# Optimization experiments

Measured on AMD Instinct MI355X. Metric: run time of the kernel, lower is better.

The kernel has to match this reference:

```python
import jax, jax.numpy as jnp
import numpy as np


def _adaptive_pool_mat(n_in, n_out):
    # torch AdaptiveAvgPool2d bin edges: start=floor(i*n_in/n_out), end=ceil((i+1)*n_in/n_out)
    M = np.zeros((n_out, n_in), np.float32)
    for i in range(n_out):
        s = (i * n_in) // n_out
        e = -(-((i + 1) * n_in) // n_out)
        M[i, s:e] = 1.0 / (e - s)
    return jnp.asarray(M)


def _bilinear_mat(n_out, n_in):
    # torch F.interpolate bilinear, align_corners=False, as a (n_out, n_in) matrix
    M = np.zeros((n_out, n_in), np.float32)
    scale = n_in / n_out
    for i in range(n_out):
        src = max((i + 0.5) * scale - 0.5, 0.0)
        i0 = min(int(np.floor(src)), n_in - 1)
        w = src - i0
        i1 = min(i0 + 1, n_in - 1)
        M[i, i0] += 1.0 - w
        M[i, i1] += w
    return jnp.asarray(M)


def _bn(x, g, b, m, v):
    # inference-mode BatchNorm2d over channel axis 1 of (B,C,H,W)
    inv = g / jnp.sqrt(v + 1e-5)
    return x * inv[None, :, None, None] + (b - m * inv)[None, :, None, None]


def _selective_scan(u, delta, A, Bs, Cs, D):
    # u, delta: (B,K,Di,L); A: (K,Di,N); Bs, Cs: (B,K,N,L); D: (K,Di)
    def step(h, inp):
        u_l, d_l, B_l, C_l = inp  # (B,K,Di), (B,K,Di), (B,K,N), (B,K,N)
        h = h * jnp.exp(d_l[..., None] * A) + (d_l * u_l)[..., None] * B_l[:, :, None, :]
        return h, jnp.einsum('bkdn,bkn->bkd', h, C_l)

    h0 = jnp.zeros(u.shape[:3] + (A.shape[-1],), u.dtype)
    xs = (u.transpose(3, 0, 1, 2), delta.transpose(3, 0, 1, 2),
          Bs.transpose(3, 0, 1, 2), Cs.transpose(3, 0, 1, 2))
    _, ys = jax.lax.scan(step, h0, xs)  # ys: (L,B,K,Di)
    return ys.transpose(1, 2, 3, 0) + D[None, :, :, None] * u


def _ss2d(x, in_proj_w, conv_w, conv_b, x_proj_w, dt_w, dt_b, A_logs, Ds, ln_g, ln_b, out_proj_w):
    # x: (B,H,W,d_model); VMamba SS2D with K=4 scan directions
    B, H, W, _ = x.shape
    K, N = 4, 16
    R = dt_w.shape[-1]
    Di = in_proj_w.shape[0] // 2
    xz = jnp.einsum('bhwc,ec->bhwe', x, in_proj_w)
    xi, z = jnp.split(xz, 2, axis=-1)
    xc = xi.transpose(0, 3, 1, 2)  # (B,Di,H,W)
    xc = jax.lax.conv_general_dilated(xc, conv_w, (1, 1), [(1, 1), (1, 1)],
                                      dimension_numbers=('NCHW', 'OIHW', 'NCHW'),
                                      feature_group_count=Di)
    xc = jax.nn.silu(xc + conv_b[None, :, None, None])
    L = H * W
    x_hw = xc.reshape(B, Di, L)
    x_wh = xc.transpose(0, 1, 3, 2).reshape(B, Di, L)
    xs2 = jnp.stack([x_hw, x_wh], axis=1)
    xs4 = jnp.concatenate([xs2, jnp.flip(xs2, axis=-1)], axis=1)  # (B,4,Di,L)
    x_dbl = jnp.einsum('bkdl,kcd->bkcl', xs4, x_proj_w)
    dts, Bm, Cm = jnp.split(x_dbl, [R, R + N], axis=2)
    delta = jax.nn.softplus(jnp.einsum('bkrl,kdr->bkdl', dts, dt_w) + dt_b[None, :, :, None])
    A = -jnp.exp(A_logs).reshape(K, Di, N)
    out_y = _selective_scan(xs4, delta, A, Bm, Cm, Ds.reshape(K, Di))  # (B,4,Di,L)
    inv_y = jnp.flip(out_y[:, 2:4], axis=-1)
    wh_y = out_y[:, 1].reshape(B, Di, W, H).transpose(0, 1, 3, 2).reshape(B, Di, L)
    invwh_y = inv_y[:, 1].reshape(B, Di, W, H).transpose(0, 1, 3, 2).reshape(B, Di, L)
    y = out_y[:, 0] + inv_y[:, 0] + wh_y + invwh_y  # (B,Di,L)
    y = y.transpose(0, 2, 1).reshape(B, H, W, Di)
    mu = jnp.mean(y, -1, keepdims=True)
    var = jnp.var(y, -1, keepdims=True)
    y = (y - mu) / jnp.sqrt(var + 1e-5) * ln_g + ln_b  # out_norm (LayerNorm)
    y = y * jax.nn.silu(z)
    return jnp.einsum('bhwd,cd->bhwc', y, out_proj_w)


def _forward(x, pool_w, pool_b, bn_g, bn_b, bn_m, bn_v, in_proj_w, conv_w, conv_b,
             x_proj_w, dt_w, dt_b, A_logs, Ds, ln_g, ln_b, out_proj_w,
             cbr_w, cbr_b, cbr_g, cbr_beta, cbr_m, cbr_v):
    B, C, H, W = x.shape
    pool_scales = [1, 5, 9, 13]  # generate_arithmetic_sequence(1, 16, 4)
    outs = [x]
    # pool layer 0: conv1x1 -> BN -> ReLU -> global avg pool -> upsample (constant)
    y0 = jnp.einsum('bchw,dc->bdhw', x, pool_w[0]) + pool_b[0][None, :, None, None]
    y0 = jax.nn.relu(_bn(y0, bn_g[0], bn_b[0], bn_m[0], bn_v[0]))
    y0 = jnp.mean(y0, axis=(2, 3), keepdims=True)
    outs.append(jnp.broadcast_to(y0, (B, y0.shape[1], H, W)))
    # pool layers 1..3: adaptive avg pool -> conv1x1 -> BN -> ReLU -> bilinear upsample
    for i, s in enumerate(pool_scales[1:], start=1):
        Mh, Mw = _adaptive_pool_mat(H, s), _adaptive_pool_mat(W, s)
        p = jnp.einsum('bchw,ph,qw->bcpq', x, Mh, Mw)
        p = jnp.einsum('bcpq,dc->bdpq', p, pool_w[i]) + pool_b[i][None, :, None, None]
        p = jax.nn.relu(_bn(p, bn_g[i], bn_b[i], bn_m[i], bn_v[i]))
        Uh, Uw = _bilinear_mat(H, s), _bilinear_mat(W, s)
        outs.append(jnp.einsum('bcpq,hp,wq->bchw', p, Uh, Uw))
    feat = jnp.concatenate(outs, axis=1)  # (B, dim*4 + in_chs = 1024, H, W)
    y = _ss2d(feat.transpose(0, 2, 3, 1), in_proj_w, conv_w, conv_b, x_proj_w,
              dt_w, dt_b, A_logs, Ds, ln_g, ln_b, out_proj_w)
    y = y.transpose(0, 3, 1, 2)
    # cbr: conv1x1 -> BN -> GELU
    y = jnp.einsum('bchw,dc->bdhw', y, cbr_w) + cbr_b[None, :, None, None]
    y = _bn(y, cbr_g, cbr_beta, cbr_m, cbr_v)
    return jax.nn.gelu(y, approximate=False)


def setup_inputs():
    key = jax.random.key(0)
    ks = jax.random.split(key, 20)
    B, C, H, W = 4, 512, 16, 16
    dim, P = 128, 4
    dm = dim * P + C            # 1024
    Di, K, N, R = 2 * dm, 4, 16, dm // 16  # 2048, 4, 16, 64
    f = jax.random.normal
    return {
        'x': f(ks[0], (B, C, H, W), jnp.float32),
        'pool_w': f(ks[1], (P, dim, C), jnp.float32) * 0.05,
        'pool_b': f(ks[2], (P, dim), jnp.float32) * 0.05,
        'bn_g': jnp.ones((P, dim), jnp.float32),
        'bn_b': jnp.zeros((P, dim), jnp.float32),
        'bn_m': f(ks[3], (P, dim), jnp.float32) * 0.1,
        'bn_v': jax.random.uniform(ks[4], (P, dim), jnp.float32, 0.5, 1.5),
        'in_proj_w': f(ks[5], (2 * Di, dm), jnp.float32) * 0.02,
        'conv_w': f(ks[6], (Di, 1, 3, 3), jnp.float32) * 0.1,
        'conv_b': f(ks[7], (Di,), jnp.float32) * 0.05,
        'x_proj_w': f(ks[8], (K, R + 2 * N, Di), jnp.float32) * 0.02,
        'dt_w': f(ks[9], (K, Di, R), jnp.float32) * 0.05,
        'dt_b': f(ks[10], (K, Di), jnp.float32) * 0.1,
        'A_logs': jax.random.uniform(ks[11], (K * Di, N), jnp.float32),
        'Ds': f(ks[12], (K * Di,), jnp.float32) * 0.1,
        'ln_g': jnp.ones((Di,), jnp.float32),
        'ln_b': jnp.zeros((Di,), jnp.float32),
        'out_proj_w': f(ks[13], (dm, Di), jnp.float32) * 0.02,
        'cbr_w': f(ks[14], (dim, dm), jnp.float32) * 0.05,
        'cbr_b': f(ks[15], (dim,), jnp.float32) * 0.05,
        'cbr_g': jnp.ones((dim,), jnp.float32),
        'cbr_beta': jnp.zeros((dim,), jnp.float32),
        'cbr_m': f(ks[16], (dim,), jnp.float32) * 0.1,
        'cbr_v': jax.random.uniform(ks[17], (dim,), jnp.float32, 0.5, 1.5),
    }


def reference(x, pool_w, pool_b, bn_g, bn_b, bn_m, bn_v, in_proj_w, conv_w, conv_b,
              x_proj_w, dt_w, dt_b, A_logs, Ds, ln_g, ln_b, out_proj_w,
              cbr_w, cbr_b, cbr_g, cbr_beta, cbr_m, cbr_v):
    return _forward(x, pool_w, pool_b, bn_g, bn_b, bn_m, bn_v, in_proj_w, conv_w, conv_b,
                    x_proj_w, dt_w, dt_b, A_logs, Ds, ln_g, ln_b, out_proj_w,
                    cbr_w, cbr_b, cbr_g, cbr_beta, cbr_m, cbr_v)
```

## Files before the change

### kernel.cpp

```cpp
#include <hip/hip_runtime.h>
#include <hip/hip_bf16.h>
#include <math.h>

#define Bsz 4
#define Cin 512
#define Hh 16
#define Ww 16
#define Lsp 256
#define DIM 128
#define DM 1024
#define DI 2048
#define KK 4
#define NST 16
#define RR 64
#define PW 384
#define NCH 4
#define CHUNK 64

#define OFF_FEAT    0u
#define SZ_FEAT     (Bsz*Lsp*DM)
#define OFF_POOLED  (OFF_FEAT + SZ_FEAT)
#define SZ_POOLED   (Bsz*Cin*275)
#define OFF_PCONV   (OFF_POOLED + SZ_POOLED)
#define SZ_PCONV    (Bsz*275*DIM)
#define OFF_Y0M     (OFF_PCONV + SZ_PCONV)
#define SZ_Y0M      (Bsz*DIM)
#define OFF_XZ      (OFF_Y0M + SZ_Y0M)
#define SZ_XZ       (Bsz*Lsp*2*DI)
#define OFF_XCT     (OFF_XZ + SZ_XZ)
#define SZ_XCT      (Bsz*Lsp*DI)
#define OFF_XDBL    (OFF_XCT + SZ_XCT)
#define SZ_XDBL     (Bsz*Lsp*PW)
#define OFF_DELTA   (OFF_XDBL + SZ_XDBL)
#define SZ_DELTA    (Bsz*KK*Lsp*DI)
#define OFF_OUTY    (OFF_DELTA + SZ_DELTA)
#define SZ_OUTY     (Bsz*KK*Lsp*DI)
#define OFF_YG      (OFF_OUTY + SZ_OUTY)
#define SZ_YG       (Bsz*Lsp*DI)
#define OFF_O1      (OFF_YG + SZ_YG)
#define SZ_O1       (Bsz*Lsp*DM)
#define OFF_O2      (OFF_O1 + SZ_O1)
#define SZ_O2       (Bsz*Lsp*DIM)
#define WS_FLOATS   (OFF_O2 + SZ_O2)

typedef __attribute__((ext_vector_type(8))) short short8;
typedef __attribute__((ext_vector_type(4))) float f32x4;

__device__ __forceinline__ short f2bf(float x) {
  __hip_bfloat16 h = __float2bfloat16(x);
  short s;
  __builtin_memcpy(&s, &h, 2);
  return s;
}
__device__ __forceinline__ float bf2f(short s) {
  unsigned u = ((unsigned)(unsigned short)s) << 16;
  float f;
  __builtin_memcpy(&f, &u, 4);
  return f;
}

__global__ __launch_bounds__(256) void f2bf5_kernel(
    const float* __restrict__ s0, short* __restrict__ d0,
    const float* __restrict__ s1, short* __restrict__ d1,
    const float* __restrict__ s2, short* __restrict__ d2,
    const float* __restrict__ s3, short* __restrict__ d3,
    const float* __restrict__ s4, short* __restrict__ d4) {
  int blk = blockIdx.x;
  const float* src; short* dst; int base;
  if (blk < 2048)      { src = s0; dst = d0; base = blk; }
  else if (blk < 2432) { src = s1; dst = d1; base = blk - 2048; }
  else if (blk < 3456) { src = s2; dst = d2; base = blk - 2432; }
  else if (blk < 3520) { src = s3; dst = d3; base = blk - 3456; }
  else                 { src = s4; dst = d4; base = blk - 3520; }
  int i = (base*256 + threadIdx.x)*8;
  float4 a = *(const float4*)(src + i);
  float4 b = *(const float4*)(src + i + 4);
  short8 o;
  o[0]=f2bf(a.x); o[1]=f2bf(a.y); o[2]=f2bf(a.z); o[3]=f2bf(a.w);
  o[4]=f2bf(b.x); o[5]=f2bf(b.y); o[6]=f2bf(b.z); o[7]=f2bf(b.w);
  *(short8*)(dst + i) = o;
}

__global__ __launch_bounds__(256) void pool0_kernel(
    const float* __restrict__ x, const float* __restrict__ pw, const float* __restrict__ pb,
    const float* __restrict__ g, const float* __restrict__ bb,
    const float* __restrict__ m, const float* __restrict__ v, float* __restrict__ y0m) {
  int bd = blockIdx.x;
  int b = bd >> 7, d = bd & 127;
  int l = threadIdx.x;
  const float* xb = x + (b*Cin)*Lsp + l;
  const float* w = pw + d*Cin;
  float a0 = 0.f, a1 = 0.f, a2 = 0.f, a3 = 0.f;
  #pragma unroll 4
  for (int c = 0; c < Cin; c += 4) {
    float4 wv = *(const float4*)(w + c);
    a0 += xb[(c+0)*Lsp] * wv.x;
    a1 += xb[(c+1)*Lsp] * wv.y;
    a2 += xb[(c+2)*Lsp] * wv.z;
    a3 += xb[(c+3)*Lsp] * wv.w;
  }
  float s = (a0 + a1) + (a2 + a3) + pb[d];
  float inv = g[d] * rsqrtf(v[d] + 1e-5f);
  s = s*inv + (bb[d] - m[d]*inv);
  s = fmaxf(s, 0.f);
  __shared__ float red[256];
  red[l] = s; __syncthreads();
  for (int off = 128; off > 0; off >>= 1) {
    if (l < off) red[l] += red[l+off];
    __syncthreads();
  }
  if (l == 0) y0m[bd] = red[0] * (1.f/256.f);
}

__device__ __forceinline__ void decode_pos(int pos, int& s, int& pp, int& qq, int& layer) {
  if (pos < 25)       { s = 5;  layer = 1; int t = pos;       pp = t/5;  qq = t%5;  }
  else if (pos < 106) { s = 9;  layer = 2; int t = pos - 25;  pp = t/9;  qq = t%9;  }
  else                { s = 13; layer = 3; int t = pos - 106; pp = t/13; qq = t%13; }
}

__global__ void pool_avg_kernel(const float* __restrict__ x, float* __restrict__ pooled) {
  int bc = blockIdx.x;
  int pos = threadIdx.x;
  if (pos >= 275) return;
  int s, pp, qq, layer;
  decode_pos(pos, s, pp, qq, layer);
  int hs = (pp*Hh)/s, he = ((pp+1)*Hh + s-1)/s;
  int ws = (qq*Ww)/s, we = ((qq+1)*Ww + s-1)/s;
  const float* xb = x + (size_t)bc*Lsp;
  float acc = 0.f;
  for (int hh = hs; hh < he; ++hh)
    for (int ww2 = ws; ww2 < we; ++ww2)
      acc += xb[hh*Ww + ww2];
  pooled[(size_t)bc*275 + pos] = acc / (float)((he-hs)*(we-ws));
}

__global__ void pconv_kernel(const float* __restrict__ pooled, const float* __restrict__ pw,
    const float* __restrict__ pb, const float* __restrict__ g, const float* __restrict__ bb,
    const float* __restrict__ m, const float* __restrict__ v, float* __restrict__ pconv) {
  int bp = blockIdx.x;
  int b = bp / 275, pos = bp % 275;
  int d = threadIdx.x;
  int s, pp, qq, layer;
  decode_pos(pos, s, pp, qq, layer);
  const float* pc = pooled + b*Cin*275 + pos;
  const float* w = pw + (layer*DIM + d)*Cin;
  float a0 = 0.f, a1 = 0.f, a2 = 0.f, a3 = 0.f;
  #pragma unroll 4
  for (int c = 0; c < Cin; c += 4) {
    float4 wv = *(const float4*)(w + c);
    a0 += pc[(c+0)*275] * wv.x;
    a1 += pc[(c+1)*275] * wv.y;
    a2 += pc[(c+2)*275] * wv.z;
    a3 += pc[(c+3)*275] * wv.w;
  }
  float acc = (a0 + a1) + (a2 + a3) + pb[layer*DIM + d];
  int ld = layer*DIM + d;
  float inv = g[ld] * rsqrtf(v[ld] + 1e-5f);
  acc = acc*inv + (bb[ld] - m[ld]*inv);
  pconv[bp*DIM + d] = fmaxf(acc, 0.f);
}

__global__ __launch_bounds__(256) void xT_kernel(const float* __restrict__ x,
    short* __restrict__ featB) {
  int b = blockIdx.z;
  int c0 = blockIdx.x*32, l0 = blockIdx.y*32;
  __shared__ float t[32][33];
  int tx = threadIdx.x & 31, ty = threadIdx.x >> 5;
  #pragma unroll
  for (int i = 0; i < 4; ++i) {
    int c = c0 + ty + i*8;
    t[ty + i*8][tx] = x[((size_t)b*Cin + c)*Lsp + l0 + tx];
  }
  __syncthreads();
  #pragma unroll
  for (int i = 0; i < 4; ++i) {
    int l = l0 + ty + i*8;
    featB[(size_t)(b*Lsp + l)*DM + c0 + tx] = f2bf(t[tx][ty + i*8]);
  }
}

__global__ __launch_bounds__(256) void feat_fill(const float* __restrict__ y0m,
    const float* __restrict__ pconv, short* __restrict__ featB) {
  int bl = blockIdx.x;
  int b = bl >> 8, l = bl & 255;
  int h = l >> 4, w = l & 15;
  for (int cc = threadIdx.x; cc < 512; cc += 256) {
    float val;
    if (cc < 128) {
      val = y0m[b*DIM + cc];
    } else {
      int i = (cc - 128) >> 7;
      int d = (cc - 128) & 127;
      int s = (i==0) ? 5 : (i==1) ? 9 : 13;
      int off = (i==0) ? 0 : (i==1) ? 25 : 106;
      float scale = (float)s / 16.f;
      float sh = fmaxf((h + 0.5f)*scale - 0.5f, 0.f);
      int h0 = min((int)sh, s-1); float wh = sh - (float)h0; int h1 = min(h0+1, s-1);
      float sw = fmaxf((w + 0.5f)*scale - 0.5f, 0.f);
      int w0 = min((int)sw, s-1); float ww2 = sw - (float)w0; int w1 = min(w0+1, s-1);
      const float* pc = pconv + b*275*DIM;
      float v00 = pc[(off + h0*s + w0)*DIM + d];
      float v01 = pc[(off + h0*s + w1)*DIM + d];
      float v10 = pc[(off + h1*s + w0)*DIM + d];
      float v11 = pc[(off + h1*s + w1)*DIM + d];
      val = (1.f-wh)*((1.f-ww2)*v00 + ww2*v01) + wh*((1.f-ww2)*v10 + ww2*v11);
    }
    featB[(size_t)bl*DM + 512 + cc] = f2bf(val);
  }
}

__device__ __forceinline__ int dir_map(int k, int l) {
  if (k == 0) return l;
  if (k == 1) return ((l & 15) << 4) | (l >> 4);
  if (k == 2) return 255 - l;
  int m = 255 - l; return ((m & 15) << 4) | (m >> 4);
}
__device__ __forceinline__ int inv_map(int k, int sp) {
  int t = ((sp & 15) << 4) | (sp >> 4);
  if (k == 0) return sp;
  if (k == 1) return t;
  if (k == 2) return 255 - sp;
  return 255 - t;
}

__device__ __forceinline__ void gload_lds16(const short* g, short* l) {
  __builtin_amdgcn_global_load_lds((const __attribute__((address_space(1))) void*)g,
                                   (__attribute__((address_space(3))) void*)l, 16, 0, 0);
}

template<int MODE>
__global__ __launch_bounds__(256) void gemm_bf(const short* __restrict__ Ag,
    const short* __restrict__ Bg, void* __restrict__ Cout, const float* __restrict__ bias,
    int M, int N, int K, int lda, int ldb,
    int azs, int bzs, unsigned czs, int ezs,
    const short* __restrict__ xcb, void* __restrict__ aux) {
  __shared__ short Als[128*64];
  __shared__ short Bls[128*64];
  int kdir = blockIdx.z;
  Ag += (size_t)kdir * azs;
  Bg += (size_t)kdir * bzs;
  size_t cz = (size_t)kdir * czs;
  if (bias) bias += (size_t)kdir * ezs;
  int tid = threadIdx.x;
  int w = tid >> 6, lane = tid & 63;
  int wm = w >> 1, wn = w & 1;
  int row0 = blockIdx.y * 128, col0 = blockIdx.x * 128;
  f32x4 acc[4][4];
  #pragma unroll
  for (int i = 0; i < 4; ++i)
    #pragma unroll
    for (int j = 0; j < 4; ++j)
      acc[i][j] = (f32x4){0.f, 0.f, 0.f, 0.f};

  for (int k0 = 0; k0 < K; k0 += 64) {
    #pragma unroll
    for (int i = 0; i < 4; ++i) {
      int slot = i*256 + w*64 + lane;
      int r = slot >> 3, pc = slot & 7;
      int c = pc ^ (r & 7);
      gload_lds16(Ag + (size_t)(row0 + r)*lda + k0 + c*8, &Als[(i*256 + w*64)*8]);
      gload_lds16(Bg + (size_t)(col0 + r)*ldb + k0 + c*8, &Bls[(i*256 + w*64)*8]);
    }
    __syncthreads();
    #pragma unroll
    for (int ks = 0; ks < 2; ++ks) {
      short8 af[4], bfr[4];
      int rsel = lane & 15, csel = ks*4 + (lane >> 4);
      #pragma unroll
      for (int mi = 0; mi < 4; ++mi) {
        int row = wm*64 + mi*16 + rsel;
        af[mi] = *(const short8*)&Als[row*64 + ((csel ^ (row & 7)) << 3)];
      }
      #pragma unroll
      for (int ni = 0; ni < 4; ++ni) {
        int row = wn*64 + ni*16 + rsel;
        bfr[ni] = *(const short8*)&Bls[row*64 + ((csel ^ (row & 7)) << 3)];
      }
      #pragma unroll
      for (int mi = 0; mi < 4; ++mi)
        #pragma unroll
        for (int ni = 0; ni < 4; ++ni)
          acc[mi][ni] = __builtin_amdgcn_mfma_f32_16x16x32_bf16(af[mi], bfr[ni], acc[mi][ni], 0, 0, 0);
    }
    __syncthreads();
  }
  #pragma unroll
  for (int mi = 0; mi < 4; ++mi) {
    int rbase = row0 + wm*64 + mi*16 + ((lane >> 4) << 2);
    #pragma unroll
    for (int ni = 0; ni < 4; ++ni) {
      int colg = col0 + wn*64 + ni*16 + (lane & 15);
      #pragma unroll
      for (int j = 0; j < 4; ++j) {
        if (MODE == 1) {
          ((short*)Cout)[(size_t)(rbase + j)*N + colg] = f2bf(acc[mi][ni][j]);
        } else if (MODE == 4) {
          int rowg = rbase + j;
          int b_ = rowg >> 8, sp_ = rowg & 255;
          int lsc = inv_map(kdir, sp_);
          float dl = acc[mi][ni][j] + bias[colg];
          dl = (dl > 20.f) ? dl : log1pf(__expf(dl));
          float ul = bf2f(xcb[(size_t)rowg*N + colg]);
          unsigned pv = ((unsigned)(unsigned short)f2bf(dl*ul) << 16)
                      |  (unsigned)(unsigned short)f2bf(dl);
          ((unsigned*)Cout)[cz + (size_t)(b_*Lsp + lsc)*N + colg] = pv;
        } else if (MODE == 5) {
          float vv = acc[mi][ni][j];
          ((float*)Cout)[(size_t)(rbase + j)*N + colg] = vv;
          ((short*)aux)[(size_t)(rbase + j)*N + colg] = f2bf(vv);
        } else {
          ((float*)Cout)[(size_t)(rbase + j)*N + colg] = acc[mi][ni][j];
        }
      }
    }
  }
}

__global__ __launch_bounds__(256) void dwconv_kernel(const short* __restrict__ xzB,
    const float* __restrict__ cw, const float* __restrict__ cb, short* __restrict__ xcB) {
  int bl = blockIdx.x;
  int b = bl >> 8, l = bl & 255;
  int h = l >> 4, w = l & 15;
  const short* xzb = xzB + (size_t)b*Lsp*(2*DI);
  for (int d = threadIdx.x; d < DI; d += 256) {
    float s = 0.f;
    #pragma unroll
    for (int dh = -1; dh <= 1; ++dh) {
      int hh = h + dh; if (hh < 0 || hh > 15) continue;
      #pragma unroll
      for (int dw = -1; dw <= 1; ++dw) {
        int ww2 = w + dw; if (ww2 < 0 || ww2 > 15) continue;
        s += bf2f(xzb[(size_t)(hh*16 + ww2)*(2*DI) + d]) * cw[d*9 + (dh+1)*3 + (dw+1)];
      }
    }
    s += cb[d];
    float r = s / (1.f + __expf(-s));
    xcB[((size_t)b*Lsp + l)*DI + d] = f2bf(r);
  }
}

__global__ __launch_bounds__(256) void ps_build(const float* __restrict__ P,
    float* __restrict__ PS) {
  int slab = blockIdx.x;
  int k = slab >> 2, b = slab & 3;
  int l = threadIdx.x;
  int sp = dir_map(k, l);
  const float* src = P + (size_t)(b*Lsp + sp)*PW + k*96 + RR;
  float* dst = PS + ((size_t)slab*Lsp + l)*32;
  #pragma unroll
  for (int n = 0; n < 32; n += 4)
    *(float4*)(dst + n) = *(const float4*)(src + n);
}

__global__ __launch_bounds__(256) void scan_pass1(const unsigned* __restrict__ pk,
    const float* __restrict__ PS, const float* __restrict__ A_logs,
    float* __restrict__ Pa, float* __restrict__ Hend) {
  int bk = blockIdx.x;
  int b = bk >> 2, k = bk & 3;
  int slab = k*Bsz + b;
  int tid = threadIdx.x;
  int wv = tid >> 6, lane = tid & 63;
  int dloc = lane >> 2, ng = lane & 3;
  int d = blockIdx.y*64 + wv*16 + dloc;
  int c = blockIdx.z;
  int n0 = ng*4;
  float A[4], h[4] = {0.f,0.f,0.f,0.f}, pa[4] = {1.f,1.f,1.f,1.f};
  #pragma unroll
  for (int j = 0; j < 4; ++j)
    A[j] = -__expf(A_logs[((size_t)k*DI + d)*NST + n0 + j]);
  const unsigned* pkp = pk + (size_t)slab*Lsp*DI;
  const float* ps  = PS + (size_t)slab*Lsp*32;
  #pragma unroll 2
  for (int l = c*CHUNK; l < (c+1)*CHUNK; ++l) {
    unsigned v = pkp[(size_t)l*DI + d];
    float dl = bf2f((short)(v & 0xffff));
    float du = bf2f((short)(v >> 16));
    float4 Bv = *(const float4*)(ps + l*32 + n0);
    float e0 = __expf(dl*A[0]); h[0] = h[0]*e0 + du*Bv.x; pa[0] *= e0;
    float e1 = __expf(dl*A[1]); h[1] = h[1]*e1 + du*Bv.y; pa[1] *= e1;
    float e2 = __expf(dl*A[2]); h[2] = h[2]*e2 + du*Bv.z; pa[2] *= e2;
    float e3 = __expf(dl*A[3]); h[3] = h[3]*e3 + du*Bv.w; pa[3] *= e3;
  }
  size_t base = ((size_t)(c*16 + bk)*DI + d)*NST + n0;
  #pragma unroll
  for (int j = 0; j < 4; ++j) {
    Pa[base + j] = pa[j];
    Hend[base + j] = h[j];
  }
}

__global__ __launch_bounds__(256) void scan_combine(const float* __restrict__ Pa,
    const float* __restrict__ Hend, float* __restrict__ Hstart) {
  int idx = blockIdx.x*256 + threadIdx.x;
  const int stride = 16*DI*NST;
  float h = 0.f;
  #pragma unroll
  for (int c = 0; c < NCH; ++c) {
    Hstart[c*stride + idx] = h;
    h = Pa[c*stride + idx]*h + Hend[c*stride + idx];
  }
}

__global__ __launch_bounds__(256) void scan_pass2(const unsigned* __restrict__ pk,
    const float* __restrict__ PS, const float* __restrict__ A_logs,
    const float* __restrict__ Hstart, short* __restrict__ oyB) {
  int bk = blockIdx.x;
  int b = bk >> 2, k = bk & 3;
  int slab = k*Bsz + b;
  int tid = threadIdx.x;
  int wv = tid >> 6, lane = tid & 63;
  int dloc = lane >> 2, ng = lane & 3;
  int d = blockIdx.y*64 + wv*16 + dloc;
  int c = blockIdx.z;
  int n0 = ng*4;
  float A[4], h[4];
  #pragma unroll
  for (int j = 0; j < 4; ++j)
    A[j] = -__expf(A_logs[((size_t)k*DI + d)*NST + n0 + j]);
  size_t hbase = ((size_t)(c*16 + bk)*DI + d)*NST + n0;
  #pragma unroll
  for (int j = 0; j < 4; ++j) h[j] = Hstart[hbase + j];
  const unsigned* pkp = pk + (size_t)slab*Lsp*DI;
  const float* ps  = PS + (size_t)slab*Lsp*32;
  short* oy = oyB + (size_t)bk*Lsp*DI;
  #pragma unroll 2
  for (int l = c*CHUNK; l < (c+1)*CHUNK; ++l) {
    unsigned v = pkp[(size_t)l*DI + d];
    float dl = bf2f((short)(v & 0xffff));
    float du = bf2f((short)(v >> 16));
    float4 Bv = *(const float4*)(ps + l*32 + n0);
    float4 Cv = *(const float4*)(ps + l*32 + 16 + n0);
    float y;
    float e0 = __expf(dl*A[0]); h[0] = h[0]*e0 + du*Bv.x; y  = h[0]*Cv.x;
    float e1 = __expf(dl*A[1]); h[1] = h[1]*e1 + du*Bv.y; y += h[1]*Cv.y;
    float e2 = __expf(dl*A[2]); h[2] = h[2]*e2 + du*Bv.z; y += h[2]*Cv.z;
    float e3 = __expf(dl*A[3]); h[3] = h[3]*e3 + du*Bv.w; y += h[3]*Cv.w;
    y += __shfl_xor(y, 1);
    y += __shfl_xor(y, 2);
    if (ng == 0) oy[(size_t)l*DI + d] = f2bf(y);
  }
}

__global__ __launch_bounds__(256) void combine_ln_kernel(const short* __restrict__ oyB,
    const short* __restrict__ xzB, const short* __restrict__ xcB,
    const float* __restrict__ Ds, const float* __restrict__ lng,
    const float* __restrict__ lnb, short* __restrict__ ygB) {
  int bl = blockIdx.x;
  int b = bl >> 8, l = bl & 255;
  int h = l >> 4, w = l & 15;
  int lT = (w << 4) | h;
  const short* oy = oyB + (size_t)b*KK*Lsp*DI;
  float vals[8];
  float sum = 0.f, sumsq = 0.f;
  #pragma unroll
  for (int i = 0; i < 8; ++i) {
    int d = threadIdx.x + i*256;
    float dsum = Ds[d] + Ds[DI + d] + Ds[2*DI + d] + Ds[3*DI + d];
    float yv = bf2f(oy[(size_t)(0*Lsp + l       )*DI + d])
             + bf2f(oy[(size_t)(2*Lsp + (255-l ))*DI + d])
             + bf2f(oy[(size_t)(1*Lsp + lT      )*DI + d])
             + bf2f(oy[(size_t)(3*Lsp + (255-lT))*DI + d])
             + bf2f(xcB[(size_t)bl*DI + d]) * dsum;
    vals[i] = yv; sum += yv; sumsq += yv*yv;
  }
  __shared__ float r1[256], r2[256];
  r1[threadIdx.x] = sum; r2[threadIdx.x] = sumsq; __syncthreads();
  for (int off = 128; off > 0; off >>= 1) {
    if (threadIdx.x < off) { r1[threadIdx.x] += r1[threadIdx.x+off]; r2[threadIdx.x] += r2[threadIdx.x+off]; }
    __syncthreads();
  }
  float mu = r1[0] * (1.f/2048.f);
  float var = r2[0] * (1.f/2048.f) - mu*mu;
  float rstd = rsqrtf(var + 1e-5f);
  const short* zrow = xzB + (size_t)bl*(2*DI) + DI;
  #pragma unroll
  for (int i = 0; i < 8; ++i) {
    int d = threadIdx.x + i*256;
    float z = bf2f(zrow[d]);
    float sz = z / (1.f + __expf(-z));
    ygB[(size_t)bl*DI + d] = f2bf(((vals[i]-mu)*rstd*lng[d] + lnb[d]) * sz);
  }
}

__global__ void cbr_epilogue(const float* __restrict__ o2, const float* __restrict__ cb,
    const float* __restrict__ g, const float* __restrict__ beta, const float* __restrict__ m_,
    const float* __restrict__ v_, float* __restrict__ out) {
  int idx = blockIdx.x*256 + threadIdx.x;
  int l = idx & 255;
  int rest = idx >> 8;
  int dd = rest & 127;
  int b = rest >> 7;
  float s = o2[((size_t)b*Lsp + l)*DIM + dd] + cb[dd];
  float inv = g[dd] * rsqrtf(v_[dd] + 1e-5f);
  s = s*inv + (beta[dd] - m_[dd]*inv);
  out[idx] = s * 0.5f * (1.f + erff(s * 0.70710678118f));
}

extern "C" void kernel_launch(void* const* d_in, const int* in_sizes, int n_in,
                              void* d_out, int out_size, void* d_ws, size_t ws_size,
                              hipStream_t stream) {
  const float* x        = (const float*)d_in[0];
  const float* pool_w   = (const float*)d_in[1];
  const float* pool_b   = (const float*)d_in[2];
  const float* bn_g     = (const float*)d_in[3];
  const float* bn_b     = (const float*)d_in[4];
  const float* bn_m     = (const float*)d_in[5];
  const float* bn_v     = (const float*)d_in[6];
  const float* in_proj_w= (const float*)d_in[7];
  const float* conv_w   = (const float*)d_in[8];
  const float* conv_b   = (const float*)d_in[9];
  const float* x_proj_w = (const float*)d_in[10];
  const float* dt_w     = (const float*)d_in[11];
  const float* dt_b     = (const float*)d_in[12];
  const float* A_logs   = (const float*)d_in[13];
  const float* Ds       = (const float*)d_in[14];
  const float* ln_g     = (const float*)d_in[15];
  const float* ln_b     = (const float*)d_in[16];
  const float* out_proj_w=(const float*)d_in[17];
  const float* cbr_w    = (const float*)d_in[18];
  const float* cbr_b    = (const float*)d_in[19];
  const float* cbr_g    = (const float*)d_in[20];
  const float* cbr_beta = (const float*)d_in[21];
  const float* cbr_m    = (const float*)d_in[22];
  const float* cbr_v    = (const float*)d_in[23];
  float* out = (float*)d_out;

  if (ws_size < (size_t)WS_FLOATS * sizeof(float)) return;
  float* ws = (float*)d_ws;
  float* pooled   = ws + OFF_POOLED;
  float* pconv    = ws + OFF_PCONV;
  float* y0m      = ws + OFF_Y0M;
  float* P        = ws + OFF_XDBL;
  unsigned* pk    = (unsigned*)(ws + OFF_DELTA);
  float* o2       = ws + OFF_O2;

  short* featB = (short*)(ws + OFF_POOLED);
  float* PS    = ws + OFF_POOLED;
  short* xzB   = (short*)(ws + OFF_XZ);
  short* wInB  = (short*)(ws + OFF_DELTA);
  short* wXB   = (short*)(ws + OFF_DELTA + 2097152);
  short* wOB   = (short*)(ws + OFF_FEAT);
  short* wCB   = (short*)(ws + OFF_PCONV);
  short* xcB   = (short*)(ws + OFF_O1);
  short* oyB   = (short*)(ws + OFF_OUTY);
  float* Pa    = ws + OFF_OUTY + 4194304;
  float* Hend  = ws + OFF_OUTY + 4194304 + 2097152;
  short* dtwB  = (short*)(ws + OFF_OUTY + 4194304);
  short* PB    = (short*)(ws + OFF_OUTY + 4194304 + 262144);
  float* Hstart= ws + OFF_YG;
  short* ygB   = (short*)(ws + OFF_DELTA);
  short* o1B   = (short*)(ws + OFF_O1);

  pool0_kernel<<<Bsz*DIM, 256, 0, stream>>>(x, pool_w, pool_b, bn_g, bn_b, bn_m, bn_v, y0m);
  pool_avg_kernel<<<Bsz*Cin, 288, 0, stream>>>(x, pooled);
  pconv_kernel<<<Bsz*275, 128, 0, stream>>>(pooled, pool_w, pool_b, bn_g, bn_b, bn_m, bn_v, pconv);
  xT_kernel<<<dim3(16, 8, Bsz), 256, 0, stream>>>(x, featB);
  feat_fill<<<Bsz*Lsp, 256, 0, stream>>>(y0m, pconv, featB);

  f2bf5_kernel<<<3776, 256, 0, stream>>>(in_proj_w, wInB, x_proj_w, wXB,
      out_proj_w, wOB, cbr_w, wCB, dt_w, dtwB);

  gemm_bf<1><<<dim3(32, 8, 1), 256, 0, stream>>>(featB, wInB, xzB, nullptr,
      1024, 4096, 1024, 1024, 1024, 0, 0, 0, 0, nullptr, nullptr);

  dwconv_kernel<<<Bsz*Lsp, 256, 0, stream>>>(xzB, conv_w, conv_b, xcB);

  gemm_bf<5><<<dim3(3, 8, 1), 256, 0, stream>>>(xcB, wXB, P, nullptr,
      1024, PW, 2048, 2048, 2048, 0, 0, 0, 0, nullptr, PB);
  ps_build<<<16, 256, 0, stream>>>(P, PS);

  gemm_bf<4><<<dim3(16, 8, KK), 256, 0, stream>>>(PB, dtwB, pk, dt_b,
      1024, DI, 64, PW, RR, 96, DI*RR, (unsigned)(Bsz*Lsp*DI), DI, xcB, nullptr);

  scan_pass1<<<dim3(Bsz*KK, DI/64, NCH), 256, 0, stream>>>(pk, PS, A_logs, Pa, Hend);
  scan_combine<<<(16*DI*NST)/256, 256, 0, stream>>>(Pa, Hend, Hstart);
  scan_pass2<<<dim3(Bsz*KK, DI/64, NCH), 256, 0, stream>>>(pk, PS, A_logs, Hstart, oyB);

  combine_ln_kernel<<<Bsz*Lsp, 256, 0, stream>>>(oyB, xzB, xcB, Ds, ln_g, ln_b, ygB);

  gemm_bf<1><<<dim3(8, 8, 1), 256, 0, stream>>>(ygB, wOB, o1B, nullptr,
      1024, 1024, 2048, 2048, 2048, 0, 0, 0, 0, nullptr, nullptr);

  gemm_bf<0><<<dim3(1, 8, 1), 256, 0, stream>>>(o1B, wCB, o2, nullptr,
      1024, DIM, 1024, 1024, 1024, 0, 0, 0, 0, nullptr, nullptr);
  cbr_epilogue<<<(Bsz*DIM*Lsp)/256, 256, 0, stream>>>(o2, cbr_b, cbr_g, cbr_beta, cbr_m, cbr_v, out);
}
```

Baseline: 354.4 us.

## Emit chunk-0 scan outputs in pass one and vectorize depthwise conv

The first scan chunk starts from a zero state, so pass one now writes its outputs directly and pass two skips that chunk, launching one fewer z-slice. Per-chunk decay products are computed in closed form as exp(A * sum(delta)) instead of a running product. The depthwise conv kernel handles two channels per thread using short2 loads and stores. The chunk-0 blocks in pass one do extra work, which adds load imbalance, and the closed-form decay can differ slightly in rounding from the running product.

```diff
diff --git a/kernel.cpp b/kernel.cpp
--- a/kernel.cpp
+++ b/kernel.cpp
@@ -57,6 +57,12 @@
   float f;
   __builtin_memcpy(&f, &u, 4);
   return f;
+}
+__device__ __forceinline__ float unpack_lo(unsigned v) {
+  unsigned u = v << 16; float f; __builtin_memcpy(&f, &u, 4); return f;
+}
+__device__ __forceinline__ float unpack_hi(unsigned v) {
+  unsigned u = v & 0xffff0000u; float f; __builtin_memcpy(&f, &u, 4); return f;
 }
 
 __global__ __launch_bounds__(256) void f2bf5_kernel(
@@ -322,20 +328,26 @@
   int b = bl >> 8, l = bl & 255;
   int h = l >> 4, w = l & 15;
   const short* xzb = xzB + (size_t)b*Lsp*(2*DI);
-  for (int d = threadIdx.x; d < DI; d += 256) {
-    float s = 0.f;
+  #pragma unroll
+  for (int it = 0; it < 4; ++it) {
+    int d = (threadIdx.x + it*256)*2;
+    float s0 = cb[d], s1 = cb[d+1];
     #pragma unroll
     for (int dh = -1; dh <= 1; ++dh) {
       int hh = h + dh; if (hh < 0 || hh > 15) continue;
       #pragma unroll
       for (int dw = -1; dw <= 1; ++dw) {
         int ww2 = w + dw; if (ww2 < 0 || ww2 > 15) continue;
-        s += bf2f(xzb[(size_t)(hh*16 + ww2)*(2*DI) + d]) * cw[d*9 + (dh+1)*3 + (dw+1)];
+        int t = (dh+1)*3 + (dw+1);
+        short2 xv = *(const short2*)&xzb[(size_t)(hh*16 + ww2)*(2*DI) + d];
+        s0 += bf2f(xv.x) * cw[d*9 + t];
+        s1 += bf2f(xv.y) * cw[(d+1)*9 + t];
       }
     }
-    s += cb[d];
-    float r = s / (1.f + __expf(-s));
-    xcB[((size_t)b*Lsp + l)*DI + d] = f2bf(r);
+    float r0 = s0 / (1.f + __expf(-s0));
+    float r1 = s1 / (1.f + __expf(-s1));
+    short2 o; o.x = f2bf(r0); o.y = f2bf(r1);
+    *(short2*)&xcB[((size_t)b*Lsp + l)*DI + d] = o;
   }
 }
 
@@ -354,7 +366,7 @@
 
 __global__ __launch_bounds__(256) void scan_pass1(const unsigned* __restrict__ pk,
     const float* __restrict__ PS, const float* __restrict__ A_logs,
-    float* __restrict__ Pa, float* __restrict__ Hend) {
+    float* __restrict__ Pa, float* __restrict__ Hend, short* __restrict__ oyB) {
   int bk = blockIdx.x;
   int b = bk >> 2, k = bk & 3;
   int slab = k*Bsz + b;
@@ -364,27 +376,50 @@
   int d = blockIdx.y*64 + wv*16 + dloc;
   int c = blockIdx.z;
   int n0 = ng*4;
-  float A[4], h[4] = {0.f,0.f,0.f,0.f}, pa[4] = {1.f,1.f,1.f,1.f};
+  float A[4], h[4] = {0.f,0.f,0.f,0.f};
+  float sdl = 0.f;
   #pragma unroll
   for (int j = 0; j < 4; ++j)
     A[j] = -__expf(A_logs[((size_t)k*DI + d)*NST + n0 + j]);
   const unsigned* pkp = pk + (size_t)slab*Lsp*DI;
   const float* ps  = PS + (size_t)slab*Lsp*32;
-  #pragma unroll 2
-  for (int l = c*CHUNK; l < (c+1)*CHUNK; ++l) {
-    unsigned v = pkp[(size_t)l*DI + d];
-    float dl = bf2f((short)(v & 0xffff));
-    float du = bf2f((short)(v >> 16));
-    float4 Bv = *(const float4*)(ps + l*32 + n0);
-    float e0 = __expf(dl*A[0]); h[0] = h[0]*e0 + du*Bv.x; pa[0] *= e0;
-    float e1 = __expf(dl*A[1]); h[1] = h[1]*e1 + du*Bv.y; pa[1] *= e1;
-    float e2 = __expf(dl*A[2]); h[2] = h[2]*e2 + du*Bv.z; pa[2] *= e2;
-    float e3 = __expf(dl*A[3]); h[3] = h[3]*e3 + du*Bv.w; pa[3] *= e3;
+  if (c == 0) {
+    short* oy = oyB + (size_t)bk*Lsp*DI;
+    #pragma unroll 2
+    for (int l = 0; l < CHUNK; ++l) {
+      unsigned v = pkp[(size_t)l*DI + d];
+      float dl = unpack_lo(v);
+      float du = unpack_hi(v);
+      sdl += dl;
+      float4 Bv = *(const float4*)(ps + l*32 + n0);
+      float4 Cv = *(const float4*)(ps + l*32 + 16 + n0);
+      float y;
+      float e0 = __expf(dl*A[0]); h[0] = h[0]*e0 + du*Bv.x; y  = h[0]*Cv.x;
+      float e1 = __expf(dl*A[1]); h[1] = h[1]*e1 + du*Bv.y; y += h[1]*Cv.y;
+      float e2 = __expf(dl*A[2]); h[2] = h[2]*e2 + du*Bv.z; y += h[2]*Cv.z;
+      float e3 = __expf(dl*A[3]); h[3] = h[3]*e3 + du*Bv.w; y += h[3]*Cv.w;
+      y += __shfl_xor(y, 1);
+      y += __shfl_xor(y, 2);
+      if (ng == 0) oy[(size_t)l*DI + d] = f2bf(y);
+    }
+  } else {
+    #pragma unroll 2
+    for (int l = c*CHUNK; l < (c+1)*CHUNK; ++l) {
+      unsigned v = pkp[(size_t)l*DI + d];
+      float dl = unpack_lo(v);
+      float du = unpack_hi(v);
+      sdl += dl;
+      float4 Bv = *(const float4*)(ps + l*32 + n0);
+      float e0 = __expf(dl*A[0]); h[0] = h[0]*e0 + du*Bv.x;
+      float e1 = __expf(dl*A[1]); h[1] = h[1]*e1 + du*Bv.y;
+      float e2 = __expf(dl*A[2]); h[2] = h[2]*e2 + du*Bv.z;
+      float e3 = __expf(dl*A[3]); h[3] = h[3]*e3 + du*Bv.w;
+    }
   }
   size_t base = ((size_t)(c*16 + bk)*DI + d)*NST + n0;
   #pragma unroll
   for (int j = 0; j < 4; ++j) {
-    Pa[base + j] = pa[j];
+    Pa[base + j] = __expf(A[j]*sdl);
     Hend[base + j] = h[j];
   }
 }
@@ -411,7 +446,7 @@
   int wv = tid >> 6, lane = tid & 63;
   int dloc = lane >> 2, ng = lane & 3;
   int d = blockIdx.y*64 + wv*16 + dloc;
-  int c = blockIdx.z;
+  int c = blockIdx.z + 1;
   int n0 = ng*4;
   float A[4], h[4];
   #pragma unroll
@@ -426,8 +461,8 @@
   #pragma unroll 2
   for (int l = c*CHUNK; l < (c+1)*CHUNK; ++l) {
     unsigned v = pkp[(size_t)l*DI + d];
-    float dl = bf2f((short)(v & 0xffff));
-    float du = bf2f((short)(v >> 16));
+    float dl = unpack_lo(v);
+    float du = unpack_hi(v);
     float4 Bv = *(const float4*)(ps + l*32 + n0);
     float4 Cv = *(const float4*)(ps + l*32 + 16 + n0);
     float y;
@@ -572,9 +607,9 @@
   gemm_bf<4><<<dim3(16, 8, KK), 256, 0, stream>>>(PB, dtwB, pk, dt_b,
       1024, DI, 64, PW, RR, 96, DI*RR, (unsigned)(Bsz*Lsp*DI), DI, xcB, nullptr);
 
-  scan_pass1<<<dim3(Bsz*KK, DI/64, NCH), 256, 0, stream>>>(pk, PS, A_logs, Pa, Hend);
+  scan_pass1<<<dim3(Bsz*KK, DI/64, NCH), 256, 0, stream>>>(pk, PS, A_logs, Pa, Hend, oyB);
   scan_combine<<<(16*DI*NST)/256, 256, 0, stream>>>(Pa, Hend, Hstart);
-  scan_pass2<<<dim3(Bsz*KK, DI/64, NCH), 256, 0, stream>>>(pk, PS, A_logs, Hstart, oyB);
+  scan_pass2<<<dim3(Bsz*KK, DI/64, NCH-1), 256, 0, stream>>>(pk, PS, A_logs, Hstart, oyB);
 
   combine_ln_kernel<<<Bsz*Lsp, 256, 0, stream>>>(oyB, xzB, xcB, Ds, ln_g, ln_b, ygB);
 
```

Result: faster. 347.3 us (-2.0%).
